# Optimization experiments

Measured on AMD Instinct MI355X. Metric: run time of the kernel, lower is better.

## Reference

```python
import jax, jax.numpy as jnp
import numpy as np

TEMPERATURE = 0.05


def setup_inputs() -> dict:
    key = jax.random.key(0)
    k1, k2 = jax.random.split(key)
    B, D = 4096, 1024
    # scale 0.1 keeps pairwise distances O(3) so the original exp(-d/T) is sane
    text_embeddings = 0.1 * jax.random.normal(k1, (B, D), dtype=jnp.float32)
    image_embeddings = 0.1 * jax.random.normal(k2, (B, D), dtype=jnp.float32)
    positive_pairs = jnp.arange(B, dtype=jnp.int32)  # unused by the loss body
    return {
        "text_embeddings": text_embeddings,
        "image_embeddings": image_embeddings,
        "positive_pairs": positive_pairs,
    }


def _pairwise_l2(t, m):
    # ||t_i - m_j|| via GEMM expansion; [B, B]
    sq = (
        jnp.sum(t * t, axis=1, keepdims=True)
        + jnp.sum(m * m, axis=1)[None, :]
        - 2.0 * (t @ m.T)
    )
    return jnp.sqrt(jnp.maximum(sq, 0.0))


def reference(text_embeddings, image_embeddings, positive_pairs):
    # loss_i = -log( exp(-d_ii/T) / sum_{j != i} exp(-d_ij/T) )
    #        = logsumexp_{j != i}(-d_ij/T) + d_ii/T   (exact same math, stable)
    dist = _pairwise_l2(text_embeddings, image_embeddings)  # [B, B]
    logits = -dist / TEMPERATURE
    diag = jnp.diagonal(logits)  # log numerator per row
    B = logits.shape[0]
    eye = jnp.eye(B, dtype=bool)
    masked = jnp.where(eye, -jnp.inf, logits)  # exclude self-term from denom
    lse = jax.nn.logsumexp(masked, axis=1)
    return jnp.mean(lse - diag)
```

## Files before the change

kernel.cpp:

```cpp
#include <hip/hip_runtime.h>
#include <math.h>


#define NB 4096
#define ND 1024
#define LSE_BIAS 90.0f
#define A2 28.85390082f
#define C2 129.8425537f
#define LN2 0.6931471805599453f
#define SCALE1 0x7F7F7F7Fu

typedef int v8i __attribute__((ext_vector_type(8)));
typedef int int4v __attribute__((ext_vector_type(4)));
typedef float v16f __attribute__((ext_vector_type(16)));

__device__ inline void gload_lds16(const unsigned char* g, unsigned char* l) {
  __builtin_amdgcn_global_load_lds(
      (const __attribute__((address_space(1))) unsigned int*)g,
      (__attribute__((address_space(3))) unsigned int*)l, 16, 0, 0);
}

__global__ void prep_kernel(const float* __restrict__ T, const float* __restrict__ M,
                            unsigned char* __restrict__ t8, unsigned char* __restrict__ m8,
                            float* __restrict__ tn, float* __restrict__ mn,
                            float* __restrict__ out) {
  int row = blockIdx.x;
  if (row == 0 && threadIdx.x == 0) out[0] = 0.0f;
  const float* src;
  unsigned char* dst;
  float* nout;
  int r;
  if (row < NB) { src = T; dst = t8; nout = tn; r = row; }
  else          { src = M; dst = m8; nout = mn; r = row - NB; }
  float4 v = ((const float4*)(src + (size_t)r * ND))[threadIdx.x];
  float s = v.x * v.x + v.y * v.y + v.z * v.z + v.w * v.w;
  int p = __builtin_amdgcn_cvt_pk_fp8_f32(v.x, v.y, 0, false);
  p = __builtin_amdgcn_cvt_pk_fp8_f32(v.z, v.w, p, true);
  ((int*)(dst + (size_t)r * ND))[threadIdx.x] = p;
  for (int off = 32; off; off >>= 1) s += __shfl_xor(s, off);
  __shared__ float wsum[4];
  if ((threadIdx.x & 63) == 0) wsum[threadIdx.x >> 6] = s;
  __syncthreads();
  if (threadIdx.x == 0) nout[r] = wsum[0] + wsum[1] + wsum[2] + wsum[3];
}

__launch_bounds__(512, 2)
__global__ void gemm_lse_kernel(const unsigned char* __restrict__ t8,
                                const unsigned char* __restrict__ m8,
                                const float* __restrict__ tn, const float* __restrict__ mn,
                                float* __restrict__ part_s, float* __restrict__ diag) {
  __shared__ unsigned char A0[256 * 128];
  __shared__ unsigned char A1[256 * 128];
  __shared__ unsigned char B0[256 * 128];
  __shared__ unsigned char B1[256 * 128];
  int b = blockIdx.x;
  int region = b & 7, idx = b >> 3;
  int rt = ((region >> 2) << 3) | (idx & 7);
  int ct = ((region & 3) << 2) | (idx >> 3);
  int tid = threadIdx.x;
  int wave = tid >> 6, lane = tid & 63;
  int hb = lane >> 5, l31 = lane & 31;
  int wr = wave >> 2, wc = wave & 3;

  v16f acc[4][2] = {};

  int l3 = lane >> 3;
  int gc = (lane & 7) ^ l3;
  const unsigned char* gA = t8 + (size_t)(rt * 256 + wave * 32 + l3) * ND + gc * 16;
  const unsigned char* gB = m8 + (size_t)(ct * 256 + wave * 32 + l3) * ND + gc * 16;

  int sw = l31 & 7;
  int arow = (wr * 128 + l31) * 128;
  int brow = (wc * 64 + l31) * 128;

#define STAGE(DA, DB, koff)                                                  \
  do {                                                                       \
    _Pragma("unroll") for (int i = 0; i < 4; ++i) {                          \
      gload_lds16(gA + (koff) + (size_t)i * 8 * ND, DA + wave * 4096 + i * 1024); \
      gload_lds16(gB + (koff) + (size_t)i * 8 * ND, DB + wave * 4096 + i * 1024); \
    }                                                                        \
  } while (0)

#define COMPUTE(SA, SB)                                                      \
  do {                                                                       \
    _Pragma("unroll") for (int ks = 0; ks < 2; ++ks) {                       \
      int q16 = ((ks * 4 + 2 * hb) ^ sw) * 16;                               \
      v8i af[4];                                                             \
      _Pragma("unroll") for (int fr = 0; fr < 4; ++fr) {                     \
        int4v x0 = *(const int4v*)&SA[arow + fr * 4096 + q16];               \
        int4v x1 = *(const int4v*)&SA[arow + fr * 4096 + (q16 ^ 16)];        \
        af[fr] = (v8i){x0.x, x0.y, x0.z, x0.w, x1.x, x1.y, x1.z, x1.w};      \
      }                                                                      \
      __builtin_amdgcn_s_setprio(1);                                         \
      _Pragma("unroll") for (int fc = 0; fc < 2; ++fc) {                     \
        int4v y0 = *(const int4v*)&SB[brow + fc * 4096 + q16];               \
        int4v y1 = *(const int4v*)&SB[brow + fc * 4096 + (q16 ^ 16)];        \
        v8i bf = (v8i){y0.x, y0.y, y0.z, y0.w, y1.x, y1.y, y1.z, y1.w};      \
        _Pragma("unroll") for (int fr = 0; fr < 4; ++fr)                     \
          acc[fr][fc] = __builtin_amdgcn_mfma_scale_f32_32x32x64_f8f6f4(     \
              af[fr], bf, acc[fr][fc], 0, 0, 0, SCALE1, 0, SCALE1);          \
      }                                                                      \
      __builtin_amdgcn_s_setprio(0);                                         \
    }                                                                        \
  } while (0)

  STAGE(A0, B0, 0);
  __syncthreads();

#pragma unroll 1
  for (int kt2 = 0; kt2 < 4; ++kt2) {
    STAGE(A1, B1, (kt2 * 2 + 1) * 128);
    COMPUTE(A0, B0);
    __syncthreads();
    if (kt2 < 3) STAGE(A0, B0, (kt2 * 2 + 2) * 128);
    COMPUTE(A1, B1);
    __syncthreads();
  }
#undef STAGE
#undef COMPUTE

  int chunk = ct * 4 + wc;
  bool diagblk = (rt == ct);
  float mnv[2];
#pragma unroll
  for (int fc = 0; fc < 2; ++fc) mnv[fc] = mn[ct * 256 + wc * 64 + fc * 32 + l31];
#pragma unroll
  for (int fr = 0; fr < 4; ++fr) {
#pragma unroll
    for (int reg = 0; reg < 16; ++reg) {
      int row = (reg & 3) + 8 * (reg >> 2) + 4 * hb;
      int grow = rt * 256 + wr * 128 + fr * 32 + row;
      float tnr = tn[grow];
      float s = 0.0f;
#pragma unroll
      for (int fc = 0; fc < 2; ++fc) {
        float sq = fmaxf(fmaf(-2.0f, acc[fr][fc][reg], tnr + mnv[fc]), 0.0f);
        float dr = __builtin_amdgcn_sqrtf(sq);
        float e = __builtin_amdgcn_exp2f(fmaf(dr, -A2, C2));
        if (diagblk) {
          int gcol = ct * 256 + wc * 64 + fc * 32 + l31;
          if (grow == gcol) {
            diag[grow] = -20.0f * dr;
            e = 0.0f;
          }
        }
        s += e;
      }
      for (int m = 16; m; m >>= 1) s += __shfl_xor(s, m);
      if (l31 == 0) part_s[(size_t)grow * 64 + chunk] = s;
    }
  }
}

__global__ void combine_kernel(const float* __restrict__ part_s,
                               const float* __restrict__ diag, float* __restrict__ out) {
  int row = blockIdx.x * 256 + threadIdx.x;
  const float* ps = part_s + (size_t)row * 64;
  float S = 0.0f;
#pragma unroll 8
  for (int c = 0; c < 64; ++c) S += ps[c];
  float loss = (LN2 * __builtin_amdgcn_logf(S) - LSE_BIAS) - diag[row];
  for (int off = 32; off; off >>= 1) loss += __shfl_xor(loss, off);
  __shared__ float wsum[4];
  if ((threadIdx.x & 63) == 0) wsum[threadIdx.x >> 6] = loss;
  __syncthreads();
  if (threadIdx.x == 0)
    atomicAdd(out, (wsum[0] + wsum[1] + wsum[2] + wsum[3]) * (1.0f / (float)NB));
}

extern "C" void kernel_launch(void* const* d_in, const int* in_sizes, int n_in,
                              void* d_out, int out_size, void* d_ws, size_t ws_size,
                              hipStream_t stream) {
  const float* T = (const float*)d_in[0];
  const float* M = (const float*)d_in[1];
  float* out = (float*)d_out;

  unsigned char* t8 = (unsigned char*)d_ws;
  unsigned char* m8 = t8 + (size_t)NB * ND;
  float* fbase = (float*)(m8 + (size_t)NB * ND);
  float* tn = fbase;
  float* mn = tn + NB;
  float* diag = mn + NB;
  float* part_s = diag + NB;

  prep_kernel<<<2 * NB, 256, 0, stream>>>(T, M, t8, m8, tn, mn, out);
  gemm_lse_kernel<<<(NB / 256) * (NB / 256), 512, 0, stream>>>(t8, m8, tn, mn, part_s, diag);
  combine_kernel<<<NB / 256, 256, 0, stream>>>(part_s, diag, out);
}
```

Baseline: 121.7 us.

## Split K-tile loads into quarter-tile phases interleaved with MFMA compute

Replaces the two-stage double-buffered load/compute loop with an eight-phase schedule per iteration. Each phase reads LDS fragments for one quarter of the output tile, issues loads for one quarter of a future tile, waits on vmcnt and runs the MFMAs between raw s_barriers. Quarter-tile buffers are refilled as soon as their consumers finish, and the global-to-LDS row mapping changes so each issue covers a quarter of the tile. The aim is finer overlap of memory and math, at the cost of many more barriers and tricky manual vmcnt accounting that could cause races or stalls.

```diff
diff --git a/kernel.cpp b/kernel.cpp
--- a/kernel.cpp
+++ b/kernel.cpp
@@ -66,58 +66,83 @@
 
   int l3 = lane >> 3;
   int gc = (lane & 7) ^ l3;
-  const unsigned char* gA = t8 + (size_t)(rt * 256 + wave * 32 + l3) * ND + gc * 16;
-  const unsigned char* gB = m8 + (size_t)(ct * 256 + wave * 32 + l3) * ND + gc * 16;
+  const unsigned char* gA0 = t8 + (size_t)(rt * 256 + wave * 8 + l3) * ND + gc * 16;
+  const unsigned char* gB0 = m8 + (size_t)(ct * 256 + wc * 8 + l3) * ND + gc * 16;
 
   int sw = l31 & 7;
   int arow = (wr * 128 + l31) * 128;
   int brow = (wc * 64 + l31) * 128;
 
-#define STAGE(DA, DB, koff)                                                  \
-  do {                                                                       \
-    _Pragma("unroll") for (int i = 0; i < 4; ++i) {                          \
-      gload_lds16(gA + (koff) + (size_t)i * 8 * ND, DA + wave * 4096 + i * 1024); \
-      gload_lds16(gB + (koff) + (size_t)i * 8 * ND, DB + wave * 4096 + i * 1024); \
-    }                                                                        \
+#define ISSUE_A(DST, I, KOFF)                                                   \
+  do {                                                                          \
+    gload_lds16(gA0 + (size_t)((I) * 64 * ND) + (KOFF),                         \
+                DST + ((I) * 64 + wave * 8) * 128);                             \
+    gload_lds16(gA0 + (size_t)(((I) * 64 + 128) * ND) + (KOFF),                 \
+                DST + ((I) * 64 + 128 + wave * 8) * 128);                       \
   } while (0)
 
-#define COMPUTE(SA, SB)                                                      \
-  do {                                                                       \
-    _Pragma("unroll") for (int ks = 0; ks < 2; ++ks) {                       \
-      int q16 = ((ks * 4 + 2 * hb) ^ sw) * 16;                               \
-      v8i af[4];                                                             \
-      _Pragma("unroll") for (int fr = 0; fr < 4; ++fr) {                     \
-        int4v x0 = *(const int4v*)&SA[arow + fr * 4096 + q16];               \
-        int4v x1 = *(const int4v*)&SA[arow + fr * 4096 + (q16 ^ 16)];        \
-        af[fr] = (v8i){x0.x, x0.y, x0.z, x0.w, x1.x, x1.y, x1.z, x1.w};      \
-      }                                                                      \
-      __builtin_amdgcn_s_setprio(1);                                         \
-      _Pragma("unroll") for (int fc = 0; fc < 2; ++fc) {                     \
-        int4v y0 = *(const int4v*)&SB[brow + fc * 4096 + q16];               \
-        int4v y1 = *(const int4v*)&SB[brow + fc * 4096 + (q16 ^ 16)];        \
-        v8i bf = (v8i){y0.x, y0.y, y0.z, y0.w, y1.x, y1.y, y1.z, y1.w};      \
-        _Pragma("unroll") for (int fr = 0; fr < 4; ++fr)                     \
-          acc[fr][fc] = __builtin_amdgcn_mfma_scale_f32_32x32x64_f8f6f4(     \
-              af[fr], bf, acc[fr][fc], 0, 0, 0, SCALE1, 0, SCALE1);          \
-      }                                                                      \
-      __builtin_amdgcn_s_setprio(0);                                         \
-    }                                                                        \
+#define ISSUE_B(DST, J, KOFF)                                                   \
+  do {                                                                          \
+    gload_lds16(gB0 + (size_t)((wr * 64 + (J) * 32) * ND) + (KOFF),             \
+                DST + (wr * 64 + (J) * 32 + wc * 8) * 128);                     \
+    gload_lds16(gB0 + (size_t)(((2 + wr) * 64 + (J) * 32) * ND) + (KOFF),       \
+                DST + ((2 + wr) * 64 + (J) * 32 + wc * 8) * 128);               \
   } while (0)
 
-  STAGE(A0, B0, 0);
-  __syncthreads();
+#define PHASE(SA, SB, I, J, ISSUE_STMT, DO_WAIT)                                \
+  do {                                                                          \
+    v8i af_[2][2], bf_[2];                                                      \
+    _Pragma("unroll") for (int ks = 0; ks < 2; ++ks) {                          \
+      int q16 = ((ks * 4 + 2 * hb) ^ sw) * 16;                                  \
+      _Pragma("unroll") for (int f = 0; f < 2; ++f) {                           \
+        int4v x0 = *(const int4v*)&SA[arow + ((I) * 2 + f) * 4096 + q16];       \
+        int4v x1 = *(const int4v*)&SA[arow + ((I) * 2 + f) * 4096 + (q16 ^ 16)];\
+        af_[ks][f] = (v8i){x0.x, x0.y, x0.z, x0.w, x1.x, x1.y, x1.z, x1.w};     \
+      }                                                                         \
+      int4v y0 = *(const int4v*)&SB[brow + (J) * 4096 + q16];                   \
+      int4v y1 = *(const int4v*)&SB[brow + (J) * 4096 + (q16 ^ 16)];            \
+      bf_[ks] = (v8i){y0.x, y0.y, y0.z, y0.w, y1.x, y1.y, y1.z, y1.w};          \
+    }                                                                           \
+    ISSUE_STMT;                                                                 \
+    if (DO_WAIT) asm volatile("s_waitcnt vmcnt(4)" ::: "memory");               \
+    __builtin_amdgcn_s_barrier();                                               \
+    __builtin_amdgcn_s_setprio(1);                                              \
+    _Pragma("unroll") for (int ks = 0; ks < 2; ++ks)                            \
+      _Pragma("unroll") for (int f = 0; f < 2; ++f)                             \
+        acc[(I) * 2 + f][J] = __builtin_amdgcn_mfma_scale_f32_32x32x64_f8f6f4(  \
+            af_[ks][f], bf_[ks], acc[(I) * 2 + f][J], 0, 0, 0, SCALE1, 0, SCALE1); \
+    __builtin_amdgcn_s_setprio(0);                                              \
+    __builtin_amdgcn_s_barrier();                                               \
+  } while (0)
+
+  ISSUE_A(A0, 0, 0);
+  ISSUE_A(A0, 1, 0);
+  ISSUE_B(B0, 0, 0);
+  ISSUE_B(B0, 1, 0);
+  ISSUE_A(A1, 0, 128);
+  ISSUE_B(B1, 0, 128);
+  asm volatile("s_waitcnt vmcnt(4)" ::: "memory");
+  __builtin_amdgcn_s_barrier();
 
 #pragma unroll 1
   for (int kt2 = 0; kt2 < 4; ++kt2) {
-    STAGE(A1, B1, (kt2 * 2 + 1) * 128);
-    COMPUTE(A0, B0);
-    __syncthreads();
-    if (kt2 < 3) STAGE(A0, B0, (kt2 * 2 + 2) * 128);
-    COMPUTE(A1, B1);
-    __syncthreads();
+    int k1 = (2 * kt2 + 1) * 128;
+    int k2 = ((2 * kt2 + 2) * 128) & (ND - 1);
+    int k3 = ((2 * kt2 + 3) * 128) & (ND - 1);
+    PHASE(A0, B0, 0, 0, ISSUE_A(A1, 1, k1), 0);
+    PHASE(A0, B0, 0, 1, ISSUE_B(B1, 1, k1), 0);
+    PHASE(A0, B0, 1, 0, ISSUE_A(A0, 0, k2), 0);
+    PHASE(A0, B0, 1, 1, ISSUE_B(B0, 0, k2), 1);
+    PHASE(A1, B1, 0, 0, ISSUE_A(A0, 1, k2), 0);
+    PHASE(A1, B1, 0, 1, ISSUE_B(B0, 1, k2), 0);
+    PHASE(A1, B1, 1, 0, ISSUE_A(A1, 0, k3), 0);
+    PHASE(A1, B1, 1, 1, ISSUE_B(B1, 0, k3), 1);
   }
-#undef STAGE
-#undef COMPUTE
+#undef PHASE
+#undef ISSUE_A
+#undef ISSUE_B
+  asm volatile("s_waitcnt vmcnt(0)" ::: "memory");
+  __builtin_amdgcn_s_barrier();
 
   int chunk = ct * 4 + wc;
   bool diagblk = (rt == ct);
```

New measurement: 126.1 us. 1.04x slower.

## Use 4 waves per block with 128x128 per-wave tiles and B-fragment prefetch

Applied to the files above, without the earlier changes.

Shrinks the GEMM block from 8 waves to 4 waves, so each wave now computes a 128x128 sub-tile (4x4 MFMA fragments) rather than 128x64. Each wave now stages 16 global-to-LDS loads per tile instead of 8. The inner loop double-buffers B fragments in registers, and __syncthreads is replaced with an explicit vmcnt wait plus barrier. The aim is to raise register-level reuse of A/B fragments and cut LDS read traffic per MFMA, at the cost of fewer waves to hide latency and higher register pressure (launch bounds 256,1).

```diff
diff --git a/kernel.cpp b/kernel.cpp
--- a/kernel.cpp
+++ b/kernel.cpp
@@ -18,6 +18,12 @@
   __builtin_amdgcn_global_load_lds(
       (const __attribute__((address_space(1))) unsigned int*)g,
       (__attribute__((address_space(3))) unsigned int*)l, 16, 0, 0);
+}
+
+__device__ inline v8i ldfrag(const unsigned char* p0, const unsigned char* p1) {
+  int4v x0 = *(const int4v*)p0;
+  int4v x1 = *(const int4v*)p1;
+  return (v8i){x0.x, x0.y, x0.z, x0.w, x1.x, x1.y, x1.z, x1.w};
 }
 
 __global__ void prep_kernel(const float* __restrict__ T, const float* __restrict__ M,
@@ -44,7 +50,7 @@
   if (threadIdx.x == 0) nout[r] = wsum[0] + wsum[1] + wsum[2] + wsum[3];
 }
 
-__launch_bounds__(512, 2)
+__launch_bounds__(256, 1)
 __global__ void gemm_lse_kernel(const unsigned char* __restrict__ t8,
                                 const unsigned char* __restrict__ m8,
                                 const float* __restrict__ tn, const float* __restrict__ mn,
@@ -60,70 +66,74 @@
   int tid = threadIdx.x;
   int wave = tid >> 6, lane = tid & 63;
   int hb = lane >> 5, l31 = lane & 31;
-  int wr = wave >> 2, wc = wave & 3;
-
-  v16f acc[4][2] = {};
+  int wr = wave >> 1, wc = wave & 1;
+
+  v16f acc[4][4] = {};
 
   int l3 = lane >> 3;
   int gc = (lane & 7) ^ l3;
-  const unsigned char* gA = t8 + (size_t)(rt * 256 + wave * 32 + l3) * ND + gc * 16;
-  const unsigned char* gB = m8 + (size_t)(ct * 256 + wave * 32 + l3) * ND + gc * 16;
+  const unsigned char* gA0 = t8 + (size_t)(rt * 256 + wave * 8 + l3) * ND + gc * 16;
+  const unsigned char* gB0 = m8 + (size_t)(ct * 256 + wave * 8 + l3) * ND + gc * 16;
 
   int sw = l31 & 7;
   int arow = (wr * 128 + l31) * 128;
-  int brow = (wc * 64 + l31) * 128;
-
-#define STAGE(DA, DB, koff)                                                  \
-  do {                                                                       \
-    _Pragma("unroll") for (int i = 0; i < 4; ++i) {                          \
-      gload_lds16(gA + (koff) + (size_t)i * 8 * ND, DA + wave * 4096 + i * 1024); \
-      gload_lds16(gB + (koff) + (size_t)i * 8 * ND, DB + wave * 4096 + i * 1024); \
-    }                                                                        \
+  int brow = (wc * 128 + l31) * 128;
+  int q0 = ((2 * hb) ^ sw) * 16;
+  int q1 = ((4 + 2 * hb) ^ sw) * 16;
+
+#define STAGE(DA, DB, KOFF)                                                     \
+  do {                                                                          \
+    _Pragma("unroll") for (int i = 0; i < 8; ++i)                               \
+      gload_lds16(gA0 + (size_t)(i * 32) * ND + (KOFF), DA + (i * 32 + wave * 8) * 128); \
+    _Pragma("unroll") for (int i = 0; i < 8; ++i)                               \
+      gload_lds16(gB0 + (size_t)(i * 32) * ND + (KOFF), DB + (i * 32 + wave * 8) * 128); \
   } while (0)
 
-#define COMPUTE(SA, SB)                                                      \
-  do {                                                                       \
-    _Pragma("unroll") for (int ks = 0; ks < 2; ++ks) {                       \
-      int q16 = ((ks * 4 + 2 * hb) ^ sw) * 16;                               \
-      v8i af[4];                                                             \
-      _Pragma("unroll") for (int fr = 0; fr < 4; ++fr) {                     \
-        int4v x0 = *(const int4v*)&SA[arow + fr * 4096 + q16];               \
-        int4v x1 = *(const int4v*)&SA[arow + fr * 4096 + (q16 ^ 16)];        \
-        af[fr] = (v8i){x0.x, x0.y, x0.z, x0.w, x1.x, x1.y, x1.z, x1.w};      \
-      }                                                                      \
-      __builtin_amdgcn_s_setprio(1);                                         \
-      _Pragma("unroll") for (int fc = 0; fc < 2; ++fc) {                     \
-        int4v y0 = *(const int4v*)&SB[brow + fc * 4096 + q16];               \
-        int4v y1 = *(const int4v*)&SB[brow + fc * 4096 + (q16 ^ 16)];        \
-        v8i bf = (v8i){y0.x, y0.y, y0.z, y0.w, y1.x, y1.y, y1.z, y1.w};      \
-        _Pragma("unroll") for (int fr = 0; fr < 4; ++fr)                     \
-          acc[fr][fc] = __builtin_amdgcn_mfma_scale_f32_32x32x64_f8f6f4(     \
-              af[fr], bf, acc[fr][fc], 0, 0, 0, SCALE1, 0, SCALE1);          \
-      }                                                                      \
-      __builtin_amdgcn_s_setprio(0);                                         \
-    }                                                                        \
+#define AFR(SA, fr, q) ldfrag(&SA[arow + (fr) * 4096 + (q)], &SA[arow + (fr) * 4096 + ((q) ^ 16)])
+#define BFR(SB, fc, q) ldfrag(&SB[brow + (fc) * 4096 + (q)], &SB[brow + (fc) * 4096 + ((q) ^ 16)])
+
+#define BODY(SA, SB, DA, DB, KOFF, DO_STAGE)                                    \
+  do {                                                                          \
+    if (DO_STAGE) STAGE(DA, DB, KOFF);                                          \
+    v8i af0[4], af1[4];                                                         \
+    _Pragma("unroll") for (int fr = 0; fr < 4; ++fr) {                          \
+      af0[fr] = AFR(SA, fr, q0);                                                \
+      af1[fr] = AFR(SA, fr, q1);                                                \
+    }                                                                           \
+    v8i bc0 = BFR(SB, 0, q0), bc1 = BFR(SB, 0, q1);                             \
+    _Pragma("unroll") for (int fc = 0; fc < 4; ++fc) {                          \
+      v8i bn0, bn1;                                                             \
+      if (fc < 3) { bn0 = BFR(SB, fc + 1, q0); bn1 = BFR(SB, fc + 1, q1); }     \
+      _Pragma("unroll") for (int fr = 0; fr < 4; ++fr) {                        \
+        acc[fr][fc] = __builtin_amdgcn_mfma_scale_f32_32x32x64_f8f6f4(          \
+            af0[fr], bc0, acc[fr][fc], 0, 0, 0, SCALE1, 0, SCALE1);             \
+        acc[fr][fc] = __builtin_amdgcn_mfma_scale_f32_32x32x64_f8f6f4(          \
+            af1[fr], bc1, acc[fr][fc], 0, 0, 0, SCALE1, 0, SCALE1);             \
+      }                                                                         \
+      if (fc < 3) { bc0 = bn0; bc1 = bn1; }                                     \
+    }                                                                           \
+    asm volatile("s_waitcnt vmcnt(0)" ::: "memory");                            \
+    __builtin_amdgcn_s_barrier();                                               \
   } while (0)
 
   STAGE(A0, B0, 0);
-  __syncthreads();
+  asm volatile("s_waitcnt vmcnt(0)" ::: "memory");
+  __builtin_amdgcn_s_barrier();
 
 #pragma unroll 1
   for (int kt2 = 0; kt2 < 4; ++kt2) {
-    STAGE(A1, B1, (kt2 * 2 + 1) * 128);
-    COMPUTE(A0, B0);
-    __syncthreads();
-    if (kt2 < 3) STAGE(A0, B0, (kt2 * 2 + 2) * 128);
-    COMPUTE(A1, B1);
-    __syncthreads();
+    BODY(A0, B0, A1, B1, (2 * kt2 + 1) * 128, 1);
+    BODY(A1, B1, A0, B0, (2 * kt2 + 2) * 128, (kt2 < 3));
   }
+#undef BODY
 #undef STAGE
-#undef COMPUTE
-
-  int chunk = ct * 4 + wc;
+#undef AFR
+#undef BFR
+
   bool diagblk = (rt == ct);
-  float mnv[2];
-#pragma unroll
-  for (int fc = 0; fc < 2; ++fc) mnv[fc] = mn[ct * 256 + wc * 64 + fc * 32 + l31];
+  float mnv[4];
+#pragma unroll
+  for (int fc = 0; fc < 4; ++fc) mnv[fc] = mn[ct * 256 + wc * 128 + fc * 32 + l31];
 #pragma unroll
   for (int fr = 0; fr < 4; ++fr) {
 #pragma unroll
@@ -131,23 +141,27 @@
       int row = (reg & 3) + 8 * (reg >> 2) + 4 * hb;
       int grow = rt * 256 + wr * 128 + fr * 32 + row;
       float tnr = tn[grow];
-      float s = 0.0f;
-#pragma unroll
-      for (int fc = 0; fc < 2; ++fc) {
-        float sq = fmaxf(fmaf(-2.0f, acc[fr][fc][reg], tnr + mnv[fc]), 0.0f);
-        float dr = __builtin_amdgcn_sqrtf(sq);
-        float e = __builtin_amdgcn_exp2f(fmaf(dr, -A2, C2));
-        if (diagblk) {
-          int gcol = ct * 256 + wc * 64 + fc * 32 + l31;
-          if (grow == gcol) {
-            diag[grow] = -20.0f * dr;
-            e = 0.0f;
+#pragma unroll
+      for (int j = 0; j < 2; ++j) {
+        float s = 0.0f;
+#pragma unroll
+        for (int f = 0; f < 2; ++f) {
+          int fc = 2 * j + f;
+          float sq = fmaxf(fmaf(-2.0f, acc[fr][fc][reg], tnr + mnv[fc]), 0.0f);
+          float dr = __builtin_amdgcn_sqrtf(sq);
+          float e = __builtin_amdgcn_exp2f(fmaf(dr, -A2, C2));
+          if (diagblk) {
+            int gcol = ct * 256 + wc * 128 + fc * 32 + l31;
+            if (grow == gcol) {
+              diag[grow] = -20.0f * dr;
+              e = 0.0f;
+            }
           }
+          s += e;
         }
-        s += e;
+        for (int m = 16; m; m >>= 1) s += __shfl_xor(s, m);
+        if (l31 == 0) part_s[(size_t)grow * 64 + (ct * 4 + wc * 2 + j)] = s;
       }
-      for (int m = 16; m; m >>= 1) s += __shfl_xor(s, m);
-      if (l31 == 0) part_s[(size_t)grow * 64 + chunk] = s;
     }
   }
 }
@@ -184,6 +198,6 @@
   float* part_s = diag + NB;
 
   prep_kernel<<<2 * NB, 256, 0, stream>>>(T, M, t8, m8, tn, mn, out);
-  gemm_lse_kernel<<<(NB / 256) * (NB / 256), 512, 0, stream>>>(t8, m8, tn, mn, part_s, diag);
+  gemm_lse_kernel<<<(NB / 256) * (NB / 256), 256, 0, stream>>>(t8, m8, tn, mn, part_s, diag);
   combine_kernel<<<NB / 256, 256, 0, stream>>>(part_s, diag, out);
 }
```

Result: slower. 149.5 us (+22.8%).
